# Performance work log

Hardware: AMD Instinct MI355X
Metric: run time of the kernel (lower is better)

## Reference

```python
import jax, jax.numpy as jnp
import numpy as np

DIM = 1024
HEADS = 16
HEAD_DIM = DIM // HEADS
MLP_HIDDEN = int(DIM * 0.7)  # 716
EPS = 1e-5


def _ln(x, g, b):
    m = jnp.mean(x, axis=-1, keepdims=True)
    v = jnp.mean(jnp.square(x - m), axis=-1, keepdims=True)
    return (x - m) * jax.lax.rsqrt(v + EPS) * g + b


def setup_inputs() -> dict:
    key = jax.random.key(0)
    ks = jax.random.split(key, 8)
    B, N = 4, 1024
    x = jax.random.normal(ks[0], (B, N, DIM), dtype=jnp.float32)
    s = 0.02
    return {
        "x": x,
        "norm_g": jnp.ones((DIM,), jnp.float32),
        "norm_b": jnp.zeros((DIM,), jnp.float32),
        "W1": jax.random.normal(ks[1], (DIM, 3 * DIM + MLP_HIDDEN), jnp.float32) * s,
        "b1": jnp.zeros((3 * DIM + MLP_HIDDEN,), jnp.float32),
        "qn_g": jnp.ones((HEAD_DIM,), jnp.float32),
        "qn_b": jnp.zeros((HEAD_DIM,), jnp.float32),
        "kn_g": jnp.ones((HEAD_DIM,), jnp.float32),
        "kn_b": jnp.zeros((HEAD_DIM,), jnp.float32),
        "projW": jax.random.normal(ks[2], (DIM, DIM), jnp.float32) * s,
        "projb": jnp.zeros((DIM,), jnp.float32),
        "mlpW": jax.random.normal(ks[3], (MLP_HIDDEN, DIM), jnp.float32) * s,  # mlp_bias=False
        "W2": jax.random.normal(ks[4], (2 * DIM, DIM), jnp.float32) * s,
        "b2": jnp.zeros((DIM,), jnp.float32),
        "ls_g": jnp.full((DIM,), 1e-5, jnp.float32),
    }


def reference(x, norm_g, norm_b, W1, b1, qn_g, qn_b, kn_g, kn_b,
              projW, projb, mlpW, W2, b2, ls_g):
    B, N, C = x.shape
    norm_x = _ln(x, norm_g, norm_b)
    f1 = norm_x @ W1 + b1  # (B, N, 3*dim + mlp_hidden)
    qkv, mlp_hidden = f1[..., :3 * DIM], f1[..., 3 * DIM:]
    # (B, N, 3, H, hd) -> (3, B, H, N, hd)
    qkv = qkv.reshape(B, N, 3, HEADS, HEAD_DIM).transpose(2, 0, 3, 1, 4)
    q, k, v = qkv[0], qkv[1], qkv[2]
    q = _ln(q, qn_g, qn_b)
    k = _ln(k, kn_g, kn_b)
    attn = jnp.einsum('bhnd,bhmd->bhnm', q, k) * (HEAD_DIM ** -0.5)
    attn = jax.nn.softmax(attn, axis=-1)
    xo = jnp.einsum('bhnm,bhmd->bhnd', attn, v)
    xo = xo.transpose(0, 2, 1, 3).reshape(B, N, DIM)
    attn_out = xo @ projW + projb
    mlp_out = jax.nn.gelu(mlp_hidden, approximate=False) @ mlpW  # no bias
    combined = jnp.concatenate([attn_out, mlp_out], axis=-1)
    out = x + (combined @ W2 + b2) * ls_g
    return out
```

## Files before the change

### kernel.cpp

```cpp
#include <hip/hip_runtime.h>
#include <cstdint>
#include <cstddef>

typedef unsigned short u16;
typedef unsigned char u8;
typedef __attribute__((ext_vector_type(8))) u16 u16x8;
typedef __attribute__((ext_vector_type(8))) __bf16 bf16x8;
typedef __attribute__((ext_vector_type(4))) float f32x4;
typedef __attribute__((ext_vector_type(16))) float f32x16;
typedef __attribute__((ext_vector_type(4))) int i32x4;
typedef __attribute__((ext_vector_type(8))) int i32x8;

__device__ __forceinline__ u16 f2bf(float f) {
  unsigned u = __builtin_bit_cast(unsigned, f);
  return (u16)((u + 0x7FFFu + ((u >> 16) & 1u)) >> 16);
}
__device__ __forceinline__ float bf2f(u16 h) {
  return __builtin_bit_cast(float, (unsigned)h << 16);
}
__device__ __forceinline__ u8 f2fp8(float f) {
  return (u8)(__builtin_amdgcn_cvt_pk_fp8_f32(f, 0.f, 0, false) & 0xFF);
}
__device__ __forceinline__ f32x4 mfma16(u16x8 a, u16x8 b, f32x4 c) {
  return __builtin_amdgcn_mfma_f32_16x16x32_bf16(
      __builtin_bit_cast(bf16x8, a), __builtin_bit_cast(bf16x8, b), c, 0, 0, 0);
}
__device__ __forceinline__ void load_lds16(const void* g, void* l) {
  __builtin_amdgcn_global_load_lds(
      (const __attribute__((address_space(1))) void*)g,
      (__attribute__((address_space(3))) void*)l, 16, 0, 0);
}

__global__ __launch_bounds__(256) void k_pre(
    const float* __restrict__ W1, const float* __restrict__ projW,
    const float* __restrict__ mlpW, const float* __restrict__ W2,
    u8* __restrict__ W1t, u8* __restrict__ pWt, u8* __restrict__ mWt,
    u8* __restrict__ W2t, const float* __restrict__ x,
    const float* __restrict__ g, const float* __restrict__ b,
    u8* __restrict__ nx8) {
  __shared__ float t[32][33];
  __shared__ float red[8];
  const int L = blockIdx.x;
  const int tid = threadIdx.x;
  if (L < 7680) {
    const float* src;
    u8* dst;
    int R, C, dR, dC, bx, by;
    if (L < 3840) {
      src = W1; dst = W1t; R = 1024; C = 3788; dR = 1024; dC = 3840;
      bx = L % 120; by = L / 120;
    } else if (L < 4864) {
      int tq = L - 3840;
      src = projW; dst = pWt; R = 1024; C = 1024; dR = 1024; dC = 1024;
      bx = tq & 31; by = tq >> 5;
    } else if (L < 5632) {
      int tq = L - 4864;
      src = mlpW; dst = mWt; R = 716; C = 1024; dR = 768; dC = 1024;
      bx = tq & 31; by = tq >> 5;
    } else {
      int tq = L - 5632;
      src = W2; dst = W2t; R = 2048; C = 1024; dR = 2048; dC = 1024;
      bx = tq & 31; by = tq >> 5;
    }
    const int n0 = bx * 32, k0 = by * 32;
    const int tx = tid & 31, ty = tid >> 5;
#pragma unroll
    for (int j = 0; j < 4; ++j) {
      int kk = k0 + ty + 8 * j, nn = n0 + tx;
      float v = (kk < R && nn < C) ? src[(size_t)kk * C + nn] : 0.f;
      t[ty + 8 * j][tx] = v;
    }
    __syncthreads();
#pragma unroll
    for (int j = 0; j < 4; ++j) {
      int nn = n0 + ty + 8 * j, kk = k0 + tx;
      if (nn < dC && kk < dR) dst[(size_t)nn * dR + kk] = f2fp8(t[tx][ty + 8 * j]);
    }
  } else {
    const int row = L - 7680;
    float4 v = ((const float4*)(x + (size_t)row * 1024))[tid];
    float s = v.x + v.y + v.z + v.w;
    float ss = v.x * v.x + v.y * v.y + v.z * v.z + v.w * v.w;
#pragma unroll
    for (int off = 1; off < 64; off <<= 1) {
      s += __shfl_xor(s, off);
      ss += __shfl_xor(ss, off);
    }
    const int wid = tid >> 6, lane = tid & 63;
    if (lane == 0) { red[wid] = s; red[4 + wid] = ss; }
    __syncthreads();
    s = red[0] + red[1] + red[2] + red[3];
    ss = red[4] + red[5] + red[6] + red[7];
    const float mean = s * (1.f / 1024.f);
    const float var = ss * (1.f / 1024.f) - mean * mean;
    const float rstd = rsqrtf(var + 1e-5f);
    float4 gv = ((const float4*)g)[tid];
    float4 bv = ((const float4*)b)[tid];
    float y0 = (v.x - mean) * rstd * gv.x + bv.x;
    float y1 = (v.y - mean) * rstd * gv.y + bv.y;
    float y2 = (v.z - mean) * rstd * gv.z + bv.z;
    float y3 = (v.w - mean) * rstd * gv.w + bv.w;
    int pk = __builtin_amdgcn_cvt_pk_fp8_f32(y0, y1, 0, false);
    pk = __builtin_amdgcn_cvt_pk_fp8_f32(y2, y3, pk, true);
    ((int*)(nx8 + (size_t)row * 1024))[tid] = pk;
  }
}

__device__ __forceinline__ void gemm_fp8_core(const u8* __restrict__ A,
                                              const u8* __restrict__ B, int K,
                                              u8* Alds, u8* Blds,
                                              f32x16 (&acc)[2][2], int tid) {
  const int lane = tid & 63, wave = tid >> 6;
  const int h = lane >> 5, r32 = lane & 31;
  const int wrow = (wave >> 1) * 64, wcol = (wave & 1) * 64;
  const int srow0 = tid >> 2, spos = tid & 3;
  const int nk = K >> 6;
#pragma unroll
  for (int p = 0; p < 2; ++p) {
    const int row = p * 64 + srow0;
    const int c = spos ^ ((row >> 1) & 3);
    const size_t go = (size_t)row * K + c * 16;
    load_lds16(A + go, Alds + (p * 256 + tid) * 16);
    load_lds16(B + go, Blds + (p * 256 + tid) * 16);
  }
  __syncthreads();
  for (int kt = 0; kt < nk; ++kt) {
    const int cur = kt & 1;
    const u8* Ac = Alds + cur * 8192;
    const u8* Bc = Blds + cur * 8192;
    if (kt + 1 < nk) {
      u8* An = Alds + (cur ^ 1) * 8192;
      u8* Bn = Blds + (cur ^ 1) * 8192;
#pragma unroll
      for (int p = 0; p < 2; ++p) {
        const int row = p * 64 + srow0;
        const int c = spos ^ ((row >> 1) & 3);
        const size_t go = (size_t)row * K + (size_t)(kt + 1) * 64 + c * 16;
        load_lds16(A + go, An + (p * 256 + tid) * 16);
        load_lds16(B + go, Bn + (p * 256 + tid) * 16);
      }
    }
    i32x8 af[2], bf[2];
#pragma unroll
    for (int t = 0; t < 2; ++t) {
      {
        const int row = wrow + t * 32 + r32;
        const int sw = (row >> 1) & 3;
        i32x4 lo = *(const i32x4*)(Ac + row * 64 + ((2 * h) ^ sw) * 16);
        i32x4 hi = *(const i32x4*)(Ac + row * 64 + ((2 * h + 1) ^ sw) * 16);
        i32x8 a;
        a[0] = lo[0]; a[1] = lo[1]; a[2] = lo[2]; a[3] = lo[3];
        a[4] = hi[0]; a[5] = hi[1]; a[6] = hi[2]; a[7] = hi[3];
        af[t] = a;
      }
      {
        const int row = wcol + t * 32 + r32;
        const int sw = (row >> 1) & 3;
        i32x4 lo = *(const i32x4*)(Bc + row * 64 + ((2 * h) ^ sw) * 16);
        i32x4 hi = *(const i32x4*)(Bc + row * 64 + ((2 * h + 1) ^ sw) * 16);
        i32x8 b8;
        b8[0] = lo[0]; b8[1] = lo[1]; b8[2] = lo[2]; b8[3] = lo[3];
        b8[4] = hi[0]; b8[5] = hi[1]; b8[6] = hi[2]; b8[7] = hi[3];
        bf[t] = b8;
      }
    }
#pragma unroll
    for (int i = 0; i < 2; ++i)
#pragma unroll
      for (int j = 0; j < 2; ++j)
        acc[i][j] = __builtin_amdgcn_mfma_scale_f32_32x32x64_f8f6f4(
            af[i], bf[j], acc[i][j], 0, 0, 0, 0x7F7F7F7F, 0, 0x7F7F7F7F);
    __syncthreads();
  }
}

__device__ __forceinline__ void gemm_fp8_core64(const u8* __restrict__ A,
                                                const u8* __restrict__ B, int K,
                                                u8* Alds, u8* Blds,
                                                f32x16 (&acc)[2], int tid) {
  const int lane = tid & 63, wave = tid >> 6;
  const int h = lane >> 5, r32 = lane & 31;
  const int wrow = (wave >> 1) * 32, wcol = (wave & 1) * 64;
  const int nk = K >> 6;
  const int ra = tid >> 2, posa = tid & 3;
  const int ca = posa ^ ((ra >> 1) & 3);
  load_lds16(A + (size_t)ra * K + ca * 16, Alds + tid * 16);
#pragma unroll
  for (int p = 0; p < 2; ++p) {
    const int s = tid + 256 * p;
    const int r = s >> 2, pos = s & 3;
    const int c = pos ^ ((r >> 1) & 3);
    load_lds16(B + (size_t)r * K + c * 16, Blds + s * 16);
  }
  __syncthreads();
  for (int kt = 0; kt < nk; ++kt) {
    const int cur = kt & 1;
    const u8* Ac = Alds + cur * 4096;
    const u8* Bc = Blds + cur * 8192;
    if (kt + 1 < nk) {
      u8* An = Alds + (cur ^ 1) * 4096;
      u8* Bn = Blds + (cur ^ 1) * 8192;
      const size_t k1 = (size_t)(kt + 1) * 64;
      load_lds16(A + (size_t)ra * K + k1 + ca * 16, An + tid * 16);
#pragma unroll
      for (int p = 0; p < 2; ++p) {
        const int s = tid + 256 * p;
        const int r = s >> 2, pos = s & 3;
        const int c = pos ^ ((r >> 1) & 3);
        load_lds16(B + (size_t)r * K + k1 + c * 16, Bn + s * 16);
      }
    }
    i32x8 af, bf[2];
    {
      const int row = wrow + r32;
      const int sw = (row >> 1) & 3;
      i32x4 lo = *(const i32x4*)(Ac + row * 64 + ((2 * h) ^ sw) * 16);
      i32x4 hi = *(const i32x4*)(Ac + row * 64 + ((2 * h + 1) ^ sw) * 16);
      af[0] = lo[0]; af[1] = lo[1]; af[2] = lo[2]; af[3] = lo[3];
      af[4] = hi[0]; af[5] = hi[1]; af[6] = hi[2]; af[7] = hi[3];
    }
#pragma unroll
    for (int t = 0; t < 2; ++t) {
      const int row = wcol + t * 32 + r32;
      const int sw = (row >> 1) & 3;
      i32x4 lo = *(const i32x4*)(Bc + row * 64 + ((2 * h) ^ sw) * 16);
      i32x4 hi = *(const i32x4*)(Bc + row * 64 + ((2 * h + 1) ^ sw) * 16);
      i32x8 b8;
      b8[0] = lo[0]; b8[1] = lo[1]; b8[2] = lo[2]; b8[3] = lo[3];
      b8[4] = hi[0]; b8[5] = hi[1]; b8[6] = hi[2]; b8[7] = hi[3];
      bf[t] = b8;
    }
#pragma unroll
    for (int j = 0; j < 2; ++j)
      acc[j] = __builtin_amdgcn_mfma_scale_f32_32x32x64_f8f6f4(
          af, bf[j], acc[j], 0, 0, 0, 0x7F7F7F7F, 0, 0x7F7F7F7F);
    __syncthreads();
  }
}

__global__ __launch_bounds__(256) void k_gemm1(const u8* __restrict__ nx8,
                                               const u8* __restrict__ W1t,
                                               u16* __restrict__ f1,
                                               const float* __restrict__ b1) {
  __shared__ __align__(16) u8 Alds[2 * 128 * 64];
  __shared__ __align__(16) u8 Blds[2 * 128 * 64];
  const int tid = threadIdx.x, bm = blockIdx.y, bn = blockIdx.x;
  f32x16 acc[2][2];
#pragma unroll
  for (int i = 0; i < 2; ++i)
#pragma unroll
    for (int j = 0; j < 2; ++j)
#pragma unroll
      for (int r = 0; r < 16; ++r) acc[i][j][r] = 0.f;
  gemm_fp8_core(nx8 + (size_t)bm * 128 * 1024, W1t + (size_t)bn * 128 * 1024, 1024,
                Alds, Blds, acc, tid);
  const int lane = tid & 63, wave = tid >> 6;
  const int h = lane >> 5, r32 = lane & 31;
  const int wrow = (wave >> 1) * 64, wcol = (wave & 1) * 64;
#pragma unroll
  for (int i = 0; i < 2; ++i)
#pragma unroll
    for (int j = 0; j < 2; ++j) {
      const int col = bn * 128 + wcol + j * 32 + r32;
      const float bs = (col < 3788) ? b1[col] : 0.f;
#pragma unroll
      for (int r = 0; r < 16; ++r) {
        const int row = bm * 128 + wrow + i * 32 + 4 * h + (r & 3) + 8 * (r >> 2);
        f1[(size_t)row * 3840 + col] = f2bf(acc[i][j][r] + bs);
      }
    }
}

__global__ __launch_bounds__(256) void k_gemm_pm(
    const u8* __restrict__ xo, const u8* __restrict__ pWt,
    const u8* __restrict__ gel, const u8* __restrict__ mWt,
    u8* __restrict__ comb, const float* __restrict__ projb) {
  __shared__ __align__(16) u8 Alds[2 * 64 * 64];
  __shared__ __align__(16) u8 Blds[2 * 128 * 64];
  const int tid = threadIdx.x, bm = blockIdx.y, bnq = blockIdx.x;
  const u8* A;
  const u8* B;
  int K, colbase;
  const float* bias;
  if (bnq < 8) {
    A = xo + (size_t)bm * 64 * 1024;
    B = pWt + (size_t)bnq * 128 * 1024;
    K = 1024; colbase = bnq * 128; bias = projb;
  } else {
    A = gel + (size_t)bm * 64 * 768;
    B = mWt + (size_t)(bnq - 8) * 128 * 768;
    K = 768; colbase = 1024 + (bnq - 8) * 128; bias = nullptr;
  }
  f32x16 acc[2];
#pragma unroll
  for (int j = 0; j < 2; ++j)
#pragma unroll
    for (int r = 0; r < 16; ++r) acc[j][r] = 0.f;
  gemm_fp8_core64(A, B, K, Alds, Blds, acc, tid);
  const int lane = tid & 63, wave = tid >> 6;
  const int h = lane >> 5, r32 = lane & 31;
  const int wrow = (wave >> 1) * 32, wcol = (wave & 1) * 64;
#pragma unroll
  for (int j = 0; j < 2; ++j) {
    const int col = colbase + wcol + j * 32 + r32;
    const float bs = (bias != nullptr) ? bias[col] : 0.f;
#pragma unroll
    for (int r = 0; r < 16; ++r) {
      const int row = bm * 64 + wrow + 4 * h + (r & 3) + 8 * (r >> 2);
      comb[(size_t)row * 2048 + col] = f2fp8(acc[j][r] + bs);
    }
  }
}

__global__ __launch_bounds__(256) void k_gemm_fin(const u8* __restrict__ comb,
                                                  const u8* __restrict__ W2t,
                                                  float* __restrict__ out,
                                                  const float* __restrict__ b2,
                                                  const float* __restrict__ x,
                                                  const float* __restrict__ lsg) {
  __shared__ __align__(16) u8 Alds[2 * 64 * 64];
  __shared__ __align__(16) u8 Blds[2 * 128 * 64];
  const int tid = threadIdx.x, bm = blockIdx.y, bn = blockIdx.x;
  f32x16 acc[2];
#pragma unroll
  for (int j = 0; j < 2; ++j)
#pragma unroll
    for (int r = 0; r < 16; ++r) acc[j][r] = 0.f;
  gemm_fp8_core64(comb + (size_t)bm * 64 * 2048, W2t + (size_t)bn * 128 * 2048, 2048,
                  Alds, Blds, acc, tid);
  const int lane = tid & 63, wave = tid >> 6;
  const int h = lane >> 5, r32 = lane & 31;
  const int wrow = (wave >> 1) * 32, wcol = (wave & 1) * 64;
#pragma unroll
  for (int j = 0; j < 2; ++j) {
    const int col = bn * 128 + wcol + j * 32 + r32;
    const float bs = b2[col], ls = lsg[col];
#pragma unroll
    for (int r = 0; r < 16; ++r) {
      const int row = bm * 64 + wrow + 4 * h + (r & 3) + 8 * (r >> 2);
      out[(size_t)row * 1024 + col] =
          x[(size_t)row * 1024 + col] + (acc[j][r] + bs) * ls;
    }
  }
}

__global__ __launch_bounds__(256) void k_mid(const u16* __restrict__ f1,
                                             const float* __restrict__ qg,
                                             const float* __restrict__ qbb,
                                             const float* __restrict__ kg,
                                             const float* __restrict__ kbb,
                                             u16* __restrict__ q,
                                             u16* __restrict__ k,
                                             u8* __restrict__ gel,
                                             u16* __restrict__ vtb) {
  __shared__ u16 tt[32][33];
  const int tid = threadIdx.x;
  const int L = blockIdx.x;
  if (L < 4096) {
    const int row = L;
    const int rem = tid >> 3;
    const int which = rem >> 4, h = rem & 15;
    const int e8 = (tid & 7) * 8;
    u16x8 xv = *(const u16x8*)(f1 + (size_t)row * 3840 + which * 1024 + h * 64 + e8);
    float xf[8];
    float s1 = 0.f, s2 = 0.f;
#pragma unroll
    for (int e = 0; e < 8; ++e) {
      xf[e] = bf2f(xv[e]);
      s1 += xf[e];
      s2 += xf[e] * xf[e];
    }
#pragma unroll
    for (int off = 1; off < 8; off <<= 1) {
      s1 += __shfl_xor(s1, off);
      s2 += __shfl_xor(s2, off);
    }
    const float mean = s1 * (1.f / 64.f);
    const float var = s2 * (1.f / 64.f) - mean * mean;
    const float rstd = rsqrtf(var + 1e-5f);
    const float* g = (which == 0) ? qg : kg;
    const float* bb = (which == 0) ? qbb : kbb;
    float4 g0 = ((const float4*)g)[e8 >> 2], g1 = ((const float4*)g)[(e8 >> 2) + 1];
    float4 b0 = ((const float4*)bb)[e8 >> 2], b1 = ((const float4*)bb)[(e8 >> 2) + 1];
    float gv[8] = {g0.x, g0.y, g0.z, g0.w, g1.x, g1.y, g1.z, g1.w};
    float bv[8] = {b0.x, b0.y, b0.z, b0.w, b1.x, b1.y, b1.z, b1.w};
    u16x8 o;
#pragma unroll
    for (int e = 0; e < 8; ++e) o[e] = f2bf((xf[e] - mean) * rstd * gv[e] + bv[e]);
    const int b = row >> 10, n = row & 1023;
    u16* dst = (which == 0) ? q : k;
    *(u16x8*)(dst + ((size_t)(b * 16 + h) * 1024 + n) * 64 + e8) = o;
  } else if (L < 5632) {
    const int id = (L - 4096) * 256 + tid;
    const int row = id / 96, c8 = id - row * 96;
    u16x8 xv = *(const u16x8*)(f1 + (size_t)row * 3840 + 3072 + c8 * 8);
    float rr[8];
#pragma unroll
    for (int e = 0; e < 8; ++e) {
      const int col = c8 * 8 + e;
      rr[e] = 0.f;
      if (col < 716) {
        float xx = bf2f(xv[e]);
        rr[e] = 0.5f * xx * (1.f + erff(xx * 0.70710678118654752f));
      }
    }
    int p0 = __builtin_amdgcn_cvt_pk_fp8_f32(rr[0], rr[1], 0, false);
    p0 = __builtin_amdgcn_cvt_pk_fp8_f32(rr[2], rr[3], p0, true);
    int p1 = __builtin_amdgcn_cvt_pk_fp8_f32(rr[4], rr[5], 0, false);
    p1 = __builtin_amdgcn_cvt_pk_fp8_f32(rr[6], rr[7], p1, true);
    uint2 pk;
    pk.x = (unsigned)p0;
    pk.y = (unsigned)p1;
    *(uint2*)(gel + (size_t)row * 768 + c8 * 8) = pk;
  } else {
    const int t = L - 5632;
    const int xq = t & 1, yq = (t >> 1) & 31, z = t >> 6;
    const int b = z >> 4, h = z & 15;
    const int d0 = xq * 32, n0 = yq * 32;
    const int tx = tid & 31, ty = tid >> 5;
#pragma unroll
    for (int j = 0; j < 4; ++j)
      tt[ty + 8 * j][tx] =
          f1[(size_t)(b * 1024 + n0 + ty + 8 * j) * 3840 + 2048 + h * 64 + d0 + tx];
    __syncthreads();
#pragma unroll
    for (int j = 0; j < 4; ++j)
      vtb[(size_t)z * 65536 + (size_t)(d0 + ty + 8 * j) * 1024 + n0 + tx] =
          tt[tx][ty + 8 * j];
  }
}

__global__ __launch_bounds__(256) void k_flash(const u16* __restrict__ q,
                                               const u16* __restrict__ k,
                                               const u16* __restrict__ vt,
                                               u8* __restrict__ xo) {
  __shared__ __align__(16) u16 Kl[2][64 * 64];
  __shared__ __align__(16) u16 Vl[2][64 * 64];
  __shared__ __align__(16) u16 Pl[4 * 16 * 64];
  const int tid = threadIdx.x, wave = tid >> 6, lane = tid & 63;
  const int l15 = lane & 15, quad = lane >> 4;
  const int L = blockIdx.x;
  const int xcd = L & 7, i = L >> 3;
  const int bh = xcd * 8 + (i & 7), qt = i >> 3;
  const int qrow0 = qt * 64 + wave * 16;
  const u16* qb = q + ((size_t)bh * 1024 + qrow0) * 64;
  const u16* kb = k + (size_t)bh * 1024 * 64;
  const u16* vb = vt + (size_t)bh * 64 * 1024;
  u16* Pw = Pl + wave * 16 * 64;

  u16x8 qf[2];
#pragma unroll
  for (int kk = 0; kk < 2; ++kk)
    qf[kk] = *(const u16x8*)(qb + (size_t)l15 * 64 + (kk * 4 + quad) * 8);

  f32x4 O[4];
  float lacc[4] = {0.f, 0.f, 0.f, 0.f};
#pragma unroll
  for (int dt = 0; dt < 4; ++dt) O[dt] = f32x4{0.f, 0.f, 0.f, 0.f};

  const int pl7 = l15 & 7;
  const int r0 = tid >> 3, c0 = (tid & 7) ^ (r0 & 7);
  const int s1 = tid + 256;
  const int r1 = s1 >> 3, c1 = (s1 & 7) ^ (r1 & 7);

  load_lds16(kb + (size_t)r0 * 64 + c0 * 8, (u16*)Kl[0] + tid * 8);
  load_lds16(kb + (size_t)r1 * 64 + c1 * 8, (u16*)Kl[0] + s1 * 8);
  load_lds16(vb + (size_t)r0 * 1024 + c0 * 8, (u16*)Vl[0] + tid * 8);
  load_lds16(vb + (size_t)r1 * 1024 + c1 * 8, (u16*)Vl[0] + s1 * 8);
  __syncthreads();

  for (int kv = 0; kv < 16; ++kv) {
    const int cur = kv & 1;
    if (kv < 15) {
      const size_t ko = (size_t)(kv + 1) * 64;
      load_lds16(kb + (ko + r0) * 64 + c0 * 8, (u16*)Kl[cur ^ 1] + tid * 8);
      load_lds16(kb + (ko + r1) * 64 + c1 * 8, (u16*)Kl[cur ^ 1] + s1 * 8);
      load_lds16(vb + (size_t)r0 * 1024 + ko + c0 * 8, (u16*)Vl[cur ^ 1] + tid * 8);
      load_lds16(vb + (size_t)r1 * 1024 + ko + c1 * 8, (u16*)Vl[cur ^ 1] + s1 * 8);
    }
    const u16* Kc = (const u16*)Kl[cur];
    const u16* Vc = (const u16*)Vl[cur];
    f32x4 S[4];
#pragma unroll
    for (int j = 0; j < 4; ++j) S[j] = f32x4{0.f, 0.f, 0.f, 0.f};
    __builtin_amdgcn_s_setprio(1);
#pragma unroll
    for (int j = 0; j < 4; ++j)
#pragma unroll
      for (int kk = 0; kk < 2; ++kk) {
        const int pos = (kk * 4 + quad) ^ pl7;
        u16x8 bfr = *(const u16x8*)(Kc + (16 * j + l15) * 64 + pos * 8);
        S[j] = mfma16(qf[kk], bfr, S[j]);
      }
    __builtin_amdgcn_s_setprio(0);
#pragma unroll
    for (int j = 0; j < 4; ++j)
#pragma unroll
      for (int r = 0; r < 4; ++r) {
        float pv = __expf(S[j][r] * 0.125f);
        lacc[r] += pv;
        const int prow = quad * 4 + r;
        const int pc = 2 * j + (l15 >> 3);
        Pw[prow * 64 + (pc ^ (prow & 7)) * 8 + pl7] = f2bf(pv);
      }
    __builtin_amdgcn_s_waitcnt(0xC07F);
    __builtin_amdgcn_s_setprio(1);
#pragma unroll
    for (int c = 0; c < 2; ++c) {
      const int pos = (c * 4 + quad) ^ pl7;
      u16x8 pa = *(const u16x8*)(Pw + l15 * 64 + pos * 8);
#pragma unroll
      for (int dt = 0; dt < 4; ++dt) {
        u16x8 vf = *(const u16x8*)(Vc + (16 * dt + l15) * 64 + pos * 8);
        O[dt] = mfma16(pa, vf, O[dt]);
      }
    }
    __builtin_amdgcn_s_setprio(0);
    __syncthreads();
  }
#pragma unroll
  for (int r = 0; r < 4; ++r) {
#pragma unroll
    for (int off = 1; off < 16; off <<= 1) lacc[r] += __shfl_xor(lacc[r], off);
  }
  const int b = bh >> 4, h = bh & 15;
#pragma unroll
  for (int r = 0; r < 4; ++r) {
    const float inv = 1.f / lacc[r];
    u8* orow = xo + (size_t)(b * 1024 + qrow0 + quad * 4 + r) * 1024 + h * 64;
#pragma unroll
    for (int dt = 0; dt < 4; ++dt) orow[16 * dt + l15] = f2fp8(O[dt][r] * inv);
  }
}

extern "C" void kernel_launch(void* const* d_in, const int* in_sizes, int n_in,
                              void* d_out, int out_size, void* d_ws, size_t ws_size,
                              hipStream_t stream) {
  (void)in_sizes; (void)n_in; (void)out_size; (void)ws_size;
  const float* x      = (const float*)d_in[0];
  const float* norm_g = (const float*)d_in[1];
  const float* norm_b = (const float*)d_in[2];
  const float* W1     = (const float*)d_in[3];
  const float* b1     = (const float*)d_in[4];
  const float* qn_g   = (const float*)d_in[5];
  const float* qn_b   = (const float*)d_in[6];
  const float* kn_g   = (const float*)d_in[7];
  const float* kn_b   = (const float*)d_in[8];
  const float* projW  = (const float*)d_in[9];
  const float* projb  = (const float*)d_in[10];
  const float* mlpW   = (const float*)d_in[11];
  const float* W2     = (const float*)d_in[12];
  const float* b2     = (const float*)d_in[13];
  const float* ls_g   = (const float*)d_in[14];

  char* ws = (char*)d_ws;
  u8*  W1t8 = (u8*)(ws + 0);
  u8*  pWt8 = (u8*)(ws + 3932160);
  u8*  mWt8 = (u8*)(ws + 4980736);
  u8*  W2t8 = (u8*)(ws + 5767168);
  u8*  nx8  = (u8*)(ws + 7864320);
  u16* f1   = (u16*)(ws + 12058624);
  u16* qbuf = (u16*)(ws + 43515904);
  u16* kbuf = (u16*)(ws + 51904512);
  u16* vtb  = (u16*)(ws + 60293120);
  u8*  gel8 = (u8*)(ws + 68681728);

  k_pre<<<11776, 256, 0, stream>>>(W1, projW, mlpW, W2, W1t8, pWt8, mWt8, W2t8,
                                   x, norm_g, norm_b, nx8);
  k_gemm1<<<dim3(30, 32), 256, 0, stream>>>(nx8, W1t8, f1, b1);
  k_mid<<<9728, 256, 0, stream>>>(f1, qn_g, qn_b, kn_g, kn_b, qbuf, kbuf, gel8,
                                  vtb);
  k_flash<<<1024, 256, 0, stream>>>(qbuf, kbuf, vtb, nx8);
  k_gemm_pm<<<dim3(16, 64), 256, 0, stream>>>(nx8, pWt8, gel8, mWt8, (u8*)f1, projb);
  k_gemm_fin<<<dim3(8, 64), 256, 0, stream>>>((u8*)f1, W2t8, (float*)d_out, b2, x,
                                              ls_g);
}
```

Before: 230.9 us.

## Rewrite flash attention with 32x32 MFMA and register-resident P via permlane swap

The attention kernel moves from 16x16x32 to 32x32x16 bf16 MFMA, with each wave covering 32 query rows and blocks shrunk to two waves (128 threads). S is computed transposed (K as A operand) so the exponentiated probabilities can be packed to bf16 and rearranged with permlane32_swap directly into the A-operand layout for the PV MFMA. This removes the per-wave LDS round trip for P and the wait that went with it. The trade-offs are fewer waves per block to share each K/V tile load, and more register pressure from the 16-wide accumulators.

```diff
diff --git a/kernel.cpp b/kernel.cpp
--- a/kernel.cpp
+++ b/kernel.cpp
@@ -10,6 +10,7 @@
 typedef __attribute__((ext_vector_type(16))) float f32x16;
 typedef __attribute__((ext_vector_type(4))) int i32x4;
 typedef __attribute__((ext_vector_type(8))) int i32x8;
+typedef __attribute__((ext_vector_type(2))) int i32x2;
 
 __device__ __forceinline__ u16 f2bf(float f) {
   unsigned u = __builtin_bit_cast(unsigned, f);
@@ -24,6 +25,20 @@
 __device__ __forceinline__ f32x4 mfma16(u16x8 a, u16x8 b, f32x4 c) {
   return __builtin_amdgcn_mfma_f32_16x16x32_bf16(
       __builtin_bit_cast(bf16x8, a), __builtin_bit_cast(bf16x8, b), c, 0, 0, 0);
+}
+__device__ __forceinline__ f32x16 mfma32(u16x8 a, u16x8 b, f32x16 c) {
+  return __builtin_amdgcn_mfma_f32_32x32x16_bf16(
+      __builtin_bit_cast(bf16x8, a), __builtin_bit_cast(bf16x8, b), c, 0, 0, 0);
+}
+__device__ __forceinline__ unsigned cvtpk_bf16(float lo, float hi) {
+  unsigned r;
+  asm("v_cvt_pk_bf16_f32 %0, %1, %2" : "=v"(r) : "v"(lo), "v"(hi));
+  return r;
+}
+__device__ __forceinline__ void plswap(unsigned& a, unsigned& b) {
+  i32x2 r = __builtin_amdgcn_permlane32_swap((int)a, (int)b, false, false);
+  a = (unsigned)r[0];
+  b = (unsigned)r[1];
 }
 __device__ __forceinline__ void load_lds16(const void* g, void* l) {
   __builtin_amdgcn_global_load_lds(
@@ -430,106 +445,128 @@
   }
 }
 
-__global__ __launch_bounds__(256) void k_flash(const u16* __restrict__ q,
+__global__ __launch_bounds__(128) void k_flash(const u16* __restrict__ q,
                                                const u16* __restrict__ k,
                                                const u16* __restrict__ vt,
                                                u8* __restrict__ xo) {
   __shared__ __align__(16) u16 Kl[2][64 * 64];
   __shared__ __align__(16) u16 Vl[2][64 * 64];
-  __shared__ __align__(16) u16 Pl[4 * 16 * 64];
   const int tid = threadIdx.x, wave = tid >> 6, lane = tid & 63;
-  const int l15 = lane & 15, quad = lane >> 4;
+  const int l31 = lane & 31, h = lane >> 5;
   const int L = blockIdx.x;
   const int xcd = L & 7, i = L >> 3;
   const int bh = xcd * 8 + (i & 7), qt = i >> 3;
-  const int qrow0 = qt * 64 + wave * 16;
+  const int qrow0 = qt * 64 + wave * 32;
   const u16* qb = q + ((size_t)bh * 1024 + qrow0) * 64;
   const u16* kb = k + (size_t)bh * 1024 * 64;
   const u16* vb = vt + (size_t)bh * 64 * 1024;
-  u16* Pw = Pl + wave * 16 * 64;
-
-  u16x8 qf[2];
-#pragma unroll
-  for (int kk = 0; kk < 2; ++kk)
-    qf[kk] = *(const u16x8*)(qb + (size_t)l15 * 64 + (kk * 4 + quad) * 8);
-
-  f32x4 O[4];
-  float lacc[4] = {0.f, 0.f, 0.f, 0.f};
-#pragma unroll
-  for (int dt = 0; dt < 4; ++dt) O[dt] = f32x4{0.f, 0.f, 0.f, 0.f};
-
-  const int pl7 = l15 & 7;
-  const int r0 = tid >> 3, c0 = (tid & 7) ^ (r0 & 7);
-  const int s1 = tid + 256;
-  const int r1 = s1 >> 3, c1 = (s1 & 7) ^ (r1 & 7);
-
-  load_lds16(kb + (size_t)r0 * 64 + c0 * 8, (u16*)Kl[0] + tid * 8);
-  load_lds16(kb + (size_t)r1 * 64 + c1 * 8, (u16*)Kl[0] + s1 * 8);
-  load_lds16(vb + (size_t)r0 * 1024 + c0 * 8, (u16*)Vl[0] + tid * 8);
-  load_lds16(vb + (size_t)r1 * 1024 + c1 * 8, (u16*)Vl[0] + s1 * 8);
+
+  u16x8 qf[4];
+#pragma unroll
+  for (int ds = 0; ds < 4; ++ds)
+    qf[ds] = *(const u16x8*)(qb + (size_t)l31 * 64 + ds * 16 + h * 8);
+
+  f32x16 O[2];
+#pragma unroll
+  for (int d2 = 0; d2 < 2; ++d2)
+#pragma unroll
+    for (int r = 0; r < 16; ++r) O[d2][r] = 0.f;
+  float lacc = 0.f;
+
+  int sr[4], sc[4];
+#pragma unroll
+  for (int p = 0; p < 4; ++p) {
+    const int s = tid + 128 * p;
+    sr[p] = s >> 3;
+    sc[p] = (s & 7) ^ (sr[p] & 7);
+  }
+
+#pragma unroll
+  for (int p = 0; p < 4; ++p) {
+    const int s = tid + 128 * p;
+    load_lds16(kb + (size_t)sr[p] * 64 + sc[p] * 8, (u16*)Kl[0] + s * 8);
+    load_lds16(vb + (size_t)sr[p] * 1024 + sc[p] * 8, (u16*)Vl[0] + s * 8);
+  }
   __syncthreads();
 
   for (int kv = 0; kv < 16; ++kv) {
     const int cur = kv & 1;
     if (kv < 15) {
       const size_t ko = (size_t)(kv + 1) * 64;
-      load_lds16(kb + (ko + r0) * 64 + c0 * 8, (u16*)Kl[cur ^ 1] + tid * 8);
-      load_lds16(kb + (ko + r1) * 64 + c1 * 8, (u16*)Kl[cur ^ 1] + s1 * 8);
-      load_lds16(vb + (size_t)r0 * 1024 + ko + c0 * 8, (u16*)Vl[cur ^ 1] + tid * 8);
-      load_lds16(vb + (size_t)r1 * 1024 + ko + c1 * 8, (u16*)Vl[cur ^ 1] + s1 * 8);
+#pragma unroll
+      for (int p = 0; p < 4; ++p) {
+        const int s = tid + 128 * p;
+        load_lds16(kb + (ko + sr[p]) * 64 + sc[p] * 8, (u16*)Kl[cur ^ 1] + s * 8);
+        load_lds16(vb + (size_t)sr[p] * 1024 + ko + sc[p] * 8,
+                   (u16*)Vl[cur ^ 1] + s * 8);
+      }
     }
     const u16* Kc = (const u16*)Kl[cur];
     const u16* Vc = (const u16*)Vl[cur];
-    f32x4 S[4];
-#pragma unroll
-    for (int j = 0; j < 4; ++j) S[j] = f32x4{0.f, 0.f, 0.f, 0.f};
+
+    f32x16 S[2];
+#pragma unroll
+    for (int t2 = 0; t2 < 2; ++t2)
+#pragma unroll
+      for (int r = 0; r < 16; ++r) S[t2][r] = 0.f;
     __builtin_amdgcn_s_setprio(1);
 #pragma unroll
-    for (int j = 0; j < 4; ++j)
-#pragma unroll
-      for (int kk = 0; kk < 2; ++kk) {
-        const int pos = (kk * 4 + quad) ^ pl7;
-        u16x8 bfr = *(const u16x8*)(Kc + (16 * j + l15) * 64 + pos * 8);
-        S[j] = mfma16(qf[kk], bfr, S[j]);
-      }
+    for (int t2 = 0; t2 < 2; ++t2) {
+      const int kr = t2 * 32 + l31;
+      const int sw = kr & 7;
+#pragma unroll
+      for (int ds = 0; ds < 4; ++ds) {
+        const int pos = (ds * 2 + h) ^ sw;
+        u16x8 kf = *(const u16x8*)(Kc + kr * 64 + pos * 8);
+        S[t2] = mfma32(kf, qf[ds], S[t2]);
+      }
+    }
     __builtin_amdgcn_s_setprio(0);
-#pragma unroll
-    for (int j = 0; j < 4; ++j)
-#pragma unroll
-      for (int r = 0; r < 4; ++r) {
-        float pv = __expf(S[j][r] * 0.125f);
-        lacc[r] += pv;
-        const int prow = quad * 4 + r;
-        const int pc = 2 * j + (l15 >> 3);
-        Pw[prow * 64 + (pc ^ (prow & 7)) * 8 + pl7] = f2bf(pv);
-      }
-    __builtin_amdgcn_s_waitcnt(0xC07F);
+
+#pragma unroll
+    for (int t2 = 0; t2 < 2; ++t2)
+#pragma unroll
+      for (int r = 0; r < 16; ++r) {
+        float pv = __expf(S[t2][r] * 0.125f);
+        S[t2][r] = pv;
+        lacc += pv;
+      }
+
     __builtin_amdgcn_s_setprio(1);
 #pragma unroll
-    for (int c = 0; c < 2; ++c) {
-      const int pos = (c * 4 + quad) ^ pl7;
-      u16x8 pa = *(const u16x8*)(Pw + l15 * 64 + pos * 8);
-#pragma unroll
-      for (int dt = 0; dt < 4; ++dt) {
-        u16x8 vf = *(const u16x8*)(Vc + (16 * dt + l15) * 64 + pos * 8);
-        O[dt] = mfma16(pa, vf, O[dt]);
+    for (int m = 0; m < 4; ++m) {
+      const int t2 = m >> 1, ro = (m & 1) * 8;
+      unsigned w0 = cvtpk_bf16(S[t2][ro + 0], S[t2][ro + 1]);
+      unsigned w2 = cvtpk_bf16(S[t2][ro + 4], S[t2][ro + 5]);
+      unsigned w1 = cvtpk_bf16(S[t2][ro + 2], S[t2][ro + 3]);
+      unsigned w3 = cvtpk_bf16(S[t2][ro + 6], S[t2][ro + 7]);
+      plswap(w0, w2);
+      plswap(w1, w3);
+      i32x4 aw;
+      aw[0] = (int)w0; aw[1] = (int)w1; aw[2] = (int)w2; aw[3] = (int)w3;
+      const u16x8 pa = __builtin_bit_cast(u16x8, aw);
+#pragma unroll
+      for (int d2 = 0; d2 < 2; ++d2) {
+        const int vr = d2 * 32 + l31;
+        const int pos = (m * 2 + h) ^ (vr & 7);
+        u16x8 vf = *(const u16x8*)(Vc + vr * 64 + pos * 8);
+        O[d2] = mfma32(pa, vf, O[d2]);
       }
     }
     __builtin_amdgcn_s_setprio(0);
     __syncthreads();
   }
-#pragma unroll
-  for (int r = 0; r < 4; ++r) {
-#pragma unroll
-    for (int off = 1; off < 16; off <<= 1) lacc[r] += __shfl_xor(lacc[r], off);
-  }
-  const int b = bh >> 4, h = bh & 15;
-#pragma unroll
-  for (int r = 0; r < 4; ++r) {
-    const float inv = 1.f / lacc[r];
-    u8* orow = xo + (size_t)(b * 1024 + qrow0 + quad * 4 + r) * 1024 + h * 64;
-#pragma unroll
-    for (int dt = 0; dt < 4; ++dt) orow[16 * dt + l15] = f2fp8(O[dt][r] * inv);
+
+  lacc += __shfl_xor(lacc, 32);
+  const float inv = 1.f / lacc;
+  const int b = bh >> 4, hh = bh & 15;
+#pragma unroll
+  for (int r = 0; r < 16; ++r) {
+    const int qr = (r & 3) + 8 * (r >> 2) + 4 * h;
+    const float invr = __shfl(inv, qr);
+    u8* orow = xo + (size_t)(b * 1024 + qrow0 + qr) * 1024 + hh * 64;
+    orow[l31] = f2fp8(O[0][r] * invr);
+    orow[32 + l31] = f2fp8(O[1][r] * invr);
   }
 }
 
@@ -570,7 +607,7 @@
   k_gemm1<<<dim3(30, 32), 256, 0, stream>>>(nx8, W1t8, f1, b1);
   k_mid<<<9728, 256, 0, stream>>>(f1, qn_g, qn_b, kn_g, kn_b, qbuf, kbuf, gel8,
                                   vtb);
-  k_flash<<<1024, 256, 0, stream>>>(qbuf, kbuf, vtb, nx8);
+  k_flash<<<1024, 128, 0, stream>>>(qbuf, kbuf, vtb, nx8);
   k_gemm_pm<<<dim3(16, 64), 256, 0, stream>>>(nx8, pWt8, gel8, mWt8, (u8*)f1, projb);
   k_gemm_fin<<<dim3(8, 64), 256, 0, stream>>>((u8*)f1, W2t8, (float*)d_out, b2, x,
                                               ls_g);
```

After: 228.8 us. Within noise of the previous version (-0.9%).
